# Performance work log

Measured on AMD Instinct MI355X. Metric: run time of the kernel, lower is better.

The kernel has to match this reference:

```python
import jax, jax.numpy as jnp
import numpy as np

N_NODES = 100000
ORDER = 2


def _spmm(edge_src, edge_dst, edge_weight, x):
    # out[dst] += w * x[src]  ==  adj @ x  with adj in COO form
    msgs = edge_weight[:, None] * x[edge_src]          # [E, d]
    return jax.ops.segment_sum(msgs, edge_dst, num_segments=N_NODES)


def setup_inputs() -> dict:
    key = jax.random.key(0)
    k1, k2, k3, k4 = jax.random.split(key, 4)
    x = jax.random.normal(k1, (N_NODES, 32), dtype=jnp.float32)
    edge_src = jax.random.randint(k2, (1600000,), 0, N_NODES, dtype=jnp.int32)
    edge_dst = jax.random.randint(k3, (1600000,), 0, N_NODES, dtype=jnp.int32)
    edge_weight = jax.random.uniform(k4, (1600000,), dtype=jnp.float32)
    return {"x": x, "edge_src": edge_src, "edge_dst": edge_dst,
            "edge_weight": edge_weight}


def reference(x, edge_src, edge_dst, edge_weight):
    # SGConvolution.forward: x = spmm(adj, x) repeated `order` times
    for _ in range(ORDER):
        x = _spmm(edge_src, edge_dst, edge_weight, x)
    return x
```

## Files before the change

### kernel.cpp

```cpp
#include <hip/hip_runtime.h>

#define N_NODES 100000
#define NEDGE   1600000
#define D       32

#define BSHIFT   8
#define BNODES   256
#define NBUCKET  ((N_NODES + BNODES - 1) / BNODES)
#define NB_PAD   392
#define EPB      4096
#define EPT      (EPB / 256)
#define CBLK     ((NEDGE + EPB - 1) / EPB)
#define CAP      4608

__global__ void bucket_hist_kernel(const int* __restrict__ dst, int* __restrict__ bucket_cnt) {
    __shared__ int h[NB_PAD];
    for (int i = threadIdx.x; i < NB_PAD; i += blockDim.x) h[i] = 0;
    __syncthreads();
    for (int e = blockIdx.x * blockDim.x + threadIdx.x; e < NEDGE; e += gridDim.x * blockDim.x)
        atomicAdd(&h[dst[e] >> BSHIFT], 1);
    __syncthreads();
    for (int i = threadIdx.x; i < NB_PAD; i += blockDim.x)
        if (h[i]) atomicAdd(&bucket_cnt[i], h[i]);
}

__global__ void bucket_scan_kernel(const int* __restrict__ bucket_cnt,
                                   int* __restrict__ bucket_off, int* __restrict__ bucket_cur) {
    __shared__ int s[512];
    int tid = threadIdx.x;
    int v = (tid < NB_PAD) ? bucket_cnt[tid] : 0;
    s[tid] = v;
    __syncthreads();
    for (int o = 1; o < 512; o <<= 1) {
        int t = (tid >= o) ? s[tid - o] : 0;
        __syncthreads();
        s[tid] += t;
        __syncthreads();
    }
    if (tid < NB_PAD) {
        int excl = s[tid] - v;
        bucket_off[tid] = excl;
        bucket_cur[tid] = excl;
    }
}

__global__ __launch_bounds__(256) void bin_edges_kernel(
        const int* __restrict__ src, const int* __restrict__ dst,
        const float* __restrict__ w,
        int* __restrict__ bucket_cur, int2* __restrict__ binned) {
    __shared__ int2 sorted[EPB];
    __shared__ unsigned short bucketOf[EPB];
    __shared__ int cnt[NB_PAD];
    __shared__ int ndoff[NB_PAD];
    __shared__ int delta[NB_PAD];
    __shared__ int partial[256];

    const int tid = threadIdx.x;
    const int e0  = blockIdx.x * EPB;
    const int total = min(EPB, NEDGE - e0);

    for (int i = tid; i < NB_PAD; i += 256) cnt[i] = 0;
    __syncthreads();

    int myd[EPT];
    #pragma unroll
    for (int it = 0; it < EPT; ++it) {
        int e = e0 + it * 256 + tid;
        myd[it] = (e < NEDGE) ? dst[e] : -1;
        if (myd[it] >= 0) atomicAdd(&cnt[myd[it] >> BSHIFT], 1);
    }
    __syncthreads();

    {
        int b0 = tid * 2;
        int c0 = 0, c1 = 0, s = 0;
        if (b0 < NB_PAD) { c0 = cnt[b0]; c1 = cnt[b0 + 1]; s = c0 + c1; }
        partial[tid] = s;
        __syncthreads();
        int v = s;
        for (int o = 1; o < 256; o <<= 1) {
            int t2 = (tid >= o) ? partial[tid - o] : 0;
            __syncthreads();
            partial[tid] += t2;
            __syncthreads();
        }
        int run = partial[tid] - v;
        if (b0 < NB_PAD) {
            ndoff[b0] = run;
            if (c0 > 0) delta[b0] = atomicAdd(&bucket_cur[b0], c0) - run;
            cnt[b0] = 0;
            run += c0;
            ndoff[b0 + 1] = run;
            if (c1 > 0) delta[b0 + 1] = atomicAdd(&bucket_cur[b0 + 1], c1) - run;
            cnt[b0 + 1] = 0;
            run += c1;
        }
    }
    __syncthreads();

    #pragma unroll
    for (int it = 0; it < EPT; ++it) {
        int d = myd[it];
        if (d >= 0) {
            int e = e0 + it * 256 + tid;
            int b = d >> BSHIFT;
            int r = atomicAdd(&cnt[b], 1);
            int loc = ndoff[b] + r;
            sorted[loc]   = make_int2(src[e] | ((d & (BNODES - 1)) << 17),
                                      __float_as_int(w[e]));
            bucketOf[loc] = (unsigned short)b;
        }
    }
    __syncthreads();

    for (int i = tid; i < total; i += 256) {
        int2 v = sorted[i];
        int  b = bucketOf[i];
        binned[delta[b] + i] = v;
    }
}

__global__ __launch_bounds__(256) void build_csr_kernel(
        const int* __restrict__ bucket_off, const int* __restrict__ bucket_cnt,
        int2* __restrict__ binned, int* __restrict__ offv, int* __restrict__ deg,
        int2* __restrict__ ovf) {
    __shared__ int2 stage[CAP];
    __shared__ int2 sorted[CAP];
    __shared__ int ndcnt[BNODES];
    __shared__ int ndoff[BNODES];

    int b = blockIdx.x;
    int tid = threadIdx.x;
    int start = bucket_off[b];
    int cnt_b = bucket_cnt[b];
    bool fast = (cnt_b <= CAP);

    ndcnt[tid] = 0;
    if (fast) {
        for (int i = tid; i < cnt_b; i += 256) stage[i] = binned[start + i];
    } else {
        for (int i = tid; i < cnt_b; i += 256) ovf[i] = binned[start + i];
    }
    __syncthreads();

    if (fast) {
        for (int i = tid; i < cnt_b; i += 256)
            atomicAdd(&ndcnt[(stage[i].x >> 17) & (BNODES - 1)], 1);
    } else {
        for (int i = tid; i < cnt_b; i += 256)
            atomicAdd(&ndcnt[(ovf[i].x >> 17) & (BNODES - 1)], 1);
    }
    __syncthreads();

    int v = ndcnt[tid];
    ndoff[tid] = v;
    __syncthreads();
    for (int o = 1; o < BNODES; o <<= 1) {
        int t = (tid >= o) ? ndoff[tid - o] : 0;
        __syncthreads();
        ndoff[tid] += t;
        __syncthreads();
    }
    {
        int incl = ndoff[tid];
        __syncthreads();
        ndoff[tid] = incl - v;
        int node = b * BNODES + tid;
        if (node < N_NODES) {
            offv[node] = start + incl - v;
            deg[node]  = v;
        }
        ndcnt[tid] = 0;
    }
    __syncthreads();

    if (fast) {
        for (int i = tid; i < cnt_b; i += 256) {
            int2 p = stage[i];
            int dl = (p.x >> 17) & (BNODES - 1);
            int r = atomicAdd(&ndcnt[dl], 1);
            sorted[ndoff[dl] + r] = make_int2(p.x & 0x1FFFF, p.y);
        }
        __syncthreads();
        for (int i = tid; i < cnt_b; i += 256) binned[start + i] = sorted[i];
    } else {
        for (int i = tid; i < cnt_b; i += 256) {
            int2 p = ovf[i];
            int dl = (p.x >> 17) & (BNODES - 1);
            int r = atomicAdd(&ndcnt[dl], 1);
            binned[start + ndoff[dl] + r] = make_int2(p.x & 0x1FFFF, p.y);
        }
    }
}

__global__ void spmm_gather_kernel(const int* __restrict__ off, const int* __restrict__ deg,
                                   const int2* __restrict__ csr_sw,
                                   const float* __restrict__ x, float* __restrict__ out) {
    int gid = blockIdx.x * blockDim.x + threadIdx.x;
    if (gid >= N_NODES * 8) return;
    int node = gid >> 3;
    int c    = gid & 7;
    int start = off[node];
    int len   = deg[node];
    float4 acc = {0.f, 0.f, 0.f, 0.f};
    int k = 0;
    for (; k + 4 <= len; k += 4) {
        int2 sw0 = csr_sw[start + k];
        int2 sw1 = csr_sw[start + k + 1];
        int2 sw2 = csr_sw[start + k + 2];
        int2 sw3 = csr_sw[start + k + 3];
        const float4 xv0 = *reinterpret_cast<const float4*>(&x[(long)sw0.x * D + c * 4]);
        const float4 xv1 = *reinterpret_cast<const float4*>(&x[(long)sw1.x * D + c * 4]);
        const float4 xv2 = *reinterpret_cast<const float4*>(&x[(long)sw2.x * D + c * 4]);
        const float4 xv3 = *reinterpret_cast<const float4*>(&x[(long)sw3.x * D + c * 4]);
        float w0 = __int_as_float(sw0.y), w1 = __int_as_float(sw1.y);
        float w2 = __int_as_float(sw2.y), w3 = __int_as_float(sw3.y);
        acc.x += w0 * xv0.x; acc.y += w0 * xv0.y; acc.z += w0 * xv0.z; acc.w += w0 * xv0.w;
        acc.x += w1 * xv1.x; acc.y += w1 * xv1.y; acc.z += w1 * xv1.z; acc.w += w1 * xv1.w;
        acc.x += w2 * xv2.x; acc.y += w2 * xv2.y; acc.z += w2 * xv2.z; acc.w += w2 * xv2.w;
        acc.x += w3 * xv3.x; acc.y += w3 * xv3.y; acc.z += w3 * xv3.z; acc.w += w3 * xv3.w;
    }
    for (; k < len; ++k) {
        int2 sw = csr_sw[start + k];
        const float4 xv = *reinterpret_cast<const float4*>(&x[(long)sw.x * D + c * 4]);
        float wt = __int_as_float(sw.y);
        acc.x += wt * xv.x; acc.y += wt * xv.y; acc.z += wt * xv.z; acc.w += wt * xv.w;
    }
    *reinterpret_cast<float4*>(&out[(long)node * D + c * 4]) = acc;
}

__global__ void spmm_scatter_kernel(const int* __restrict__ src, const int* __restrict__ dst,
                                    const float* __restrict__ w, const float* __restrict__ x,
                                    float* __restrict__ out) {
    long gid = (long)blockIdx.x * blockDim.x + threadIdx.x;
    if (gid >= (long)NEDGE * 8) return;
    int e = (int)(gid >> 3);
    int c = (int)(gid & 7);
    int s = src[e], d = dst[e];
    float wt = w[e];
    const float4 xv = *reinterpret_cast<const float4*>(&x[(long)s * D + c * 4]);
    float* o = &out[(long)d * D + c * 4];
    atomicAdd(o + 0, wt * xv.x);
    atomicAdd(o + 1, wt * xv.y);
    atomicAdd(o + 2, wt * xv.z);
    atomicAdd(o + 3, wt * xv.w);
}

extern "C" void kernel_launch(void* const* d_in, const int* in_sizes, int n_in,
                              void* d_out, int out_size, void* d_ws, size_t ws_size,
                              hipStream_t stream) {
    const float* x    = (const float*)d_in[0];
    const int*   esrc = (const int*)d_in[1];
    const int*   edst = (const int*)d_in[2];
    const float* ew   = (const float*)d_in[3];
    float* out = (float*)d_out;

    char* ws = (char*)d_ws;
    const size_t y_bytes = (size_t)N_NODES * D * sizeof(float);
    const size_t n_ints  = (size_t)N_NODES * sizeof(int);
    const size_t b_ints  = (size_t)NB_PAD * sizeof(int);
    const size_t e_sw    = (size_t)NEDGE * sizeof(int2);

    size_t o = 0;
    float* y          = (float*)(ws + o); o += y_bytes;
    int2*  binned     = (int2*) (ws + o); o += e_sw;
    int*   off        = (int*)  (ws + o); o += n_ints;
    int*   deg        = (int*)  (ws + o); o += n_ints;
    int*   bucket_cnt = (int*)  (ws + o); o += b_ints;
    int*   bucket_off = (int*)  (ws + o); o += b_ints;
    int*   bucket_cur = (int*)  (ws + o); o += b_ints;

    if (ws_size < o) {
        hipMemsetAsync(y, 0, y_bytes, stream);
        hipMemsetAsync(out, 0, y_bytes, stream);
        const long total = (long)NEDGE * 8;
        const int blocks = (int)((total + 255) / 256);
        spmm_scatter_kernel<<<blocks, 256, 0, stream>>>(esrc, edst, ew, x, y);
        spmm_scatter_kernel<<<blocks, 256, 0, stream>>>(esrc, edst, ew, y, out);
        return;
    }

    hipMemsetAsync(bucket_cnt, 0, b_ints, stream);

    bucket_hist_kernel<<<256, 256, 0, stream>>>(edst, bucket_cnt);
    bucket_scan_kernel<<<1, 512, 0, stream>>>(bucket_cnt, bucket_off, bucket_cur);
    bin_edges_kernel<<<CBLK, 256, 0, stream>>>(esrc, edst, ew, bucket_cur, binned);
    build_csr_kernel<<<NBUCKET, 256, 0, stream>>>(bucket_off, bucket_cnt, binned, off, deg,
                                                  (int2*)y);

    const int gblocks = (N_NODES * 8 + 255) / 256;
    spmm_gather_kernel<<<gblocks, 256, 0, stream>>>(off, deg, binned, x, y);
    spmm_gather_kernel<<<gblocks, 256, 0, stream>>>(off, deg, binned, y, out);
}
```

Measured before the change: 126.3 us.

## Replace histogram and scan with fixed-capacity per-bucket arenas

Drops the bucket histogram, scan and memset passes by giving each destination bucket a fixed-size arena slot and initializing cursors to b*CAP. build_csr reads edges directly from global memory instead of staging them in shared memory, halving its LDS use. This removes two kernel launches and a full pass over dst. Edges beyond CAP in any bucket would be silently dropped or overwrite the neighbour arena, so correctness relies on bucket sizes staying under capacity.

```diff
diff --git a/kernel.cpp b/kernel.cpp
--- a/kernel.cpp
+++ b/kernel.cpp
@@ -11,37 +11,11 @@
 #define EPB      4096
 #define EPT      (EPB / 256)
 #define CBLK     ((NEDGE + EPB - 1) / EPB)
-#define CAP      4608
-
-__global__ void bucket_hist_kernel(const int* __restrict__ dst, int* __restrict__ bucket_cnt) {
-    __shared__ int h[NB_PAD];
-    for (int i = threadIdx.x; i < NB_PAD; i += blockDim.x) h[i] = 0;
-    __syncthreads();
-    for (int e = blockIdx.x * blockDim.x + threadIdx.x; e < NEDGE; e += gridDim.x * blockDim.x)
-        atomicAdd(&h[dst[e] >> BSHIFT], 1);
-    __syncthreads();
-    for (int i = threadIdx.x; i < NB_PAD; i += blockDim.x)
-        if (h[i]) atomicAdd(&bucket_cnt[i], h[i]);
-}
-
-__global__ void bucket_scan_kernel(const int* __restrict__ bucket_cnt,
-                                   int* __restrict__ bucket_off, int* __restrict__ bucket_cur) {
-    __shared__ int s[512];
-    int tid = threadIdx.x;
-    int v = (tid < NB_PAD) ? bucket_cnt[tid] : 0;
-    s[tid] = v;
-    __syncthreads();
-    for (int o = 1; o < 512; o <<= 1) {
-        int t = (tid >= o) ? s[tid - o] : 0;
-        __syncthreads();
-        s[tid] += t;
-        __syncthreads();
-    }
-    if (tid < NB_PAD) {
-        int excl = s[tid] - v;
-        bucket_off[tid] = excl;
-        bucket_cur[tid] = excl;
-    }
+#define CAP      5120
+
+__global__ void init_cur_kernel(int* __restrict__ bucket_cur) {
+    int i = blockIdx.x * blockDim.x + threadIdx.x;
+    if (i < NB_PAD) bucket_cur[i] = i * CAP;
 }
 
 __global__ __launch_bounds__(256) void bin_edges_kernel(
@@ -121,35 +95,22 @@
 }
 
 __global__ __launch_bounds__(256) void build_csr_kernel(
-        const int* __restrict__ bucket_off, const int* __restrict__ bucket_cnt,
-        int2* __restrict__ binned, int* __restrict__ offv, int* __restrict__ deg,
-        int2* __restrict__ ovf) {
-    __shared__ int2 stage[CAP];
+        const int* __restrict__ bucket_cur,
+        int2* __restrict__ binned, int* __restrict__ offv, int* __restrict__ deg) {
     __shared__ int2 sorted[CAP];
     __shared__ int ndcnt[BNODES];
     __shared__ int ndoff[BNODES];
 
     int b = blockIdx.x;
     int tid = threadIdx.x;
-    int start = bucket_off[b];
-    int cnt_b = bucket_cnt[b];
-    bool fast = (cnt_b <= CAP);
+    int start = b * CAP;
+    int cnt_b = min(bucket_cur[b] - start, CAP);
 
     ndcnt[tid] = 0;
-    if (fast) {
-        for (int i = tid; i < cnt_b; i += 256) stage[i] = binned[start + i];
-    } else {
-        for (int i = tid; i < cnt_b; i += 256) ovf[i] = binned[start + i];
-    }
-    __syncthreads();
-
-    if (fast) {
-        for (int i = tid; i < cnt_b; i += 256)
-            atomicAdd(&ndcnt[(stage[i].x >> 17) & (BNODES - 1)], 1);
-    } else {
-        for (int i = tid; i < cnt_b; i += 256)
-            atomicAdd(&ndcnt[(ovf[i].x >> 17) & (BNODES - 1)], 1);
-    }
+    __syncthreads();
+
+    for (int i = tid; i < cnt_b; i += 256)
+        atomicAdd(&ndcnt[(binned[start + i].x >> 17) & (BNODES - 1)], 1);
     __syncthreads();
 
     int v = ndcnt[tid];
@@ -174,23 +135,14 @@
     }
     __syncthreads();
 
-    if (fast) {
-        for (int i = tid; i < cnt_b; i += 256) {
-            int2 p = stage[i];
-            int dl = (p.x >> 17) & (BNODES - 1);
-            int r = atomicAdd(&ndcnt[dl], 1);
-            sorted[ndoff[dl] + r] = make_int2(p.x & 0x1FFFF, p.y);
-        }
-        __syncthreads();
-        for (int i = tid; i < cnt_b; i += 256) binned[start + i] = sorted[i];
-    } else {
-        for (int i = tid; i < cnt_b; i += 256) {
-            int2 p = ovf[i];
-            int dl = (p.x >> 17) & (BNODES - 1);
-            int r = atomicAdd(&ndcnt[dl], 1);
-            binned[start + ndoff[dl] + r] = make_int2(p.x & 0x1FFFF, p.y);
-        }
-    }
+    for (int i = tid; i < cnt_b; i += 256) {
+        int2 p = binned[start + i];
+        int dl = (p.x >> 17) & (BNODES - 1);
+        int r = atomicAdd(&ndcnt[dl], 1);
+        sorted[ndoff[dl] + r] = make_int2(p.x & 0x1FFFF, p.y);
+    }
+    __syncthreads();
+    for (int i = tid; i < cnt_b; i += 256) binned[start + i] = sorted[i];
 }
 
 __global__ void spmm_gather_kernel(const int* __restrict__ off, const int* __restrict__ deg,
@@ -256,18 +208,16 @@
     float* out = (float*)d_out;
 
     char* ws = (char*)d_ws;
-    const size_t y_bytes = (size_t)N_NODES * D * sizeof(float);
-    const size_t n_ints  = (size_t)N_NODES * sizeof(int);
-    const size_t b_ints  = (size_t)NB_PAD * sizeof(int);
-    const size_t e_sw    = (size_t)NEDGE * sizeof(int2);
+    const size_t y_bytes   = (size_t)N_NODES * D * sizeof(float);
+    const size_t n_ints    = (size_t)N_NODES * sizeof(int);
+    const size_t b_ints    = (size_t)NB_PAD * sizeof(int);
+    const size_t arena_sz  = (size_t)NBUCKET * CAP * sizeof(int2);
 
     size_t o = 0;
     float* y          = (float*)(ws + o); o += y_bytes;
-    int2*  binned     = (int2*) (ws + o); o += e_sw;
+    int2*  binned     = (int2*) (ws + o); o += arena_sz;
     int*   off        = (int*)  (ws + o); o += n_ints;
     int*   deg        = (int*)  (ws + o); o += n_ints;
-    int*   bucket_cnt = (int*)  (ws + o); o += b_ints;
-    int*   bucket_off = (int*)  (ws + o); o += b_ints;
     int*   bucket_cur = (int*)  (ws + o); o += b_ints;
 
     if (ws_size < o) {
@@ -280,13 +230,9 @@
         return;
     }
 
-    hipMemsetAsync(bucket_cnt, 0, b_ints, stream);
-
-    bucket_hist_kernel<<<256, 256, 0, stream>>>(edst, bucket_cnt);
-    bucket_scan_kernel<<<1, 512, 0, stream>>>(bucket_cnt, bucket_off, bucket_cur);
+    init_cur_kernel<<<2, 256, 0, stream>>>(bucket_cur);
     bin_edges_kernel<<<CBLK, 256, 0, stream>>>(esrc, edst, ew, bucket_cur, binned);
-    build_csr_kernel<<<NBUCKET, 256, 0, stream>>>(bucket_off, bucket_cnt, binned, off, deg,
-                                                  (int2*)y);
+    build_csr_kernel<<<NBUCKET, 256, 0, stream>>>(bucket_cur, binned, off, deg);
 
     const int gblocks = (N_NODES * 8 + 255) / 256;
     spmm_gather_kernel<<<gblocks, 256, 0, stream>>>(off, deg, binned, x, y);
```

Result: faster. 112.1 us (-11.3%).
